# Kernel tuning notes

Measured on AMD Instinct MI355X. Metric: run time of the kernel, lower is better.

Reference implementation:

```python
import jax, jax.numpy as jnp
import numpy as np

N, E = 50000, 1600000
FEAT, HID, HEADS = 256, 64, 2
NEG_SLOPE = 0.2


def gat_conv(x, src, dst, W, att_src, att_dst, bias, heads, out_ch):
    """PyG GATConv (concat=True, self-loops already appended to src/dst)."""
    n = x.shape[0]
    h = (x @ W).reshape(n, heads, out_ch)                      # [N,H,C]
    a_src = jnp.einsum('nhc,hc->nh', h, att_src)               # [N,H]
    a_dst = jnp.einsum('nhc,hc->nh', h, att_dst)               # [N,H]
    alpha = jax.nn.leaky_relu(a_src[src] + a_dst[dst], NEG_SLOPE)  # [E',H]
    # segment softmax over incoming edges of each dst node
    amax = jax.ops.segment_max(alpha, dst, num_segments=n)
    alpha = jnp.exp(alpha - amax[dst])
    denom = jax.ops.segment_sum(alpha, dst, num_segments=n)
    alpha = alpha / (denom[dst] + 1e-16)
    msg = h[src] * alpha[..., None]                            # [E',H,C]
    out = jax.ops.segment_sum(msg, dst, num_segments=n)        # [N,H,C]
    return out.reshape(n, heads * out_ch) + bias


def setup_inputs() -> dict:
    key = jax.random.key(0)
    ks = jax.random.split(key, 10)
    x = jax.random.normal(ks[0], (N, FEAT), dtype=jnp.float32)
    edge_index = jax.random.randint(ks[1], (2, E), 0, N, dtype=jnp.int64)
    s1 = 1.0 / np.sqrt(FEAT)
    s2 = 1.0 / np.sqrt(HID * HEADS)
    sa = 1.0 / np.sqrt(HID)
    return {
        'x': x,
        'edge_index': edge_index,
        'W1': jax.random.uniform(ks[2], (FEAT, HEADS * HID), jnp.float32, -s1, s1),
        'att_src1': jax.random.uniform(ks[3], (HEADS, HID), jnp.float32, -sa, sa),
        'att_dst1': jax.random.uniform(ks[4], (HEADS, HID), jnp.float32, -sa, sa),
        'b1': jnp.zeros((HEADS * HID,), jnp.float32),
        'W2': jax.random.uniform(ks[5], (HEADS * HID, HID), jnp.float32, -s2, s2),
        'att_src2': jax.random.uniform(ks[6], (1, HID), jnp.float32, -sa, sa),
        'att_dst2': jax.random.uniform(ks[7], (1, HID), jnp.float32, -sa, sa),
        'b2': jnp.zeros((HID,), jnp.float32),
    }


def reference(x, edge_index, W1, att_src1, att_dst1, b1, W2, att_src2, att_dst2, b2):
    n = x.shape[0]
    loop = jnp.arange(n, dtype=edge_index.dtype)
    src = jnp.concatenate([edge_index[0], loop])   # add self loops (PyG default)
    dst = jnp.concatenate([edge_index[1], loop])
    h = gat_conv(x, src, dst, W1, att_src1, att_dst1, b1, HEADS, HID)
    h = jax.nn.relu(h)  # dropout is identity in eval mode
    h = gat_conv(h, src, dst, W2, att_src2, att_dst2, b2, 1, HID)
    return jax.nn.log_softmax(h, axis=1)
```

## Files before the change

### kernel.cpp

```cpp
#include <hip/hip_runtime.h>
#include <hip/hip_bf16.h>
#include <math.h>

typedef short bf16x8 __attribute__((ext_vector_type(8)));
typedef float f32x4 __attribute__((ext_vector_type(4)));

#define BSHIFT 7
#define BWIDTH 128
#define PCHUNK 4096

__global__ void prep_kernel(int* __restrict__ bcnt,
                            const float* __restrict__ W1, const float* __restrict__ W2,
                            __hip_bfloat16* __restrict__ W1t,
                            __hip_bfloat16* __restrict__ W2t) {
    if (blockIdx.x == 0) {
        bcnt[threadIdx.x] = 0;
        bcnt[threadIdx.x + 256] = 0;
        return;
    }
    int idx = (blockIdx.x - 1) * 256 + threadIdx.x;
    const int n1 = 128 * 256;
    if (idx < n1) {
        int nn = idx >> 8, kk = idx & 255;
        W1t[idx] = __float2bfloat16(W1[kk * 128 + nn]);
    } else {
        int j = idx - n1;
        if (j < 64 * 128) {
            int nn = j >> 7, kk = j & 127;
            W2t[j] = __float2bfloat16(W2[kk * 64 + nn]);
        }
    }
}

__global__ __launch_bounds__(256) void bucket_hist(const int* __restrict__ ei, int E,
                                                   int* __restrict__ bcnt) {
    __shared__ int h[512];
    int tid = threadIdx.x;
    for (int i = tid; i < 512; i += 256) h[i] = 0;
    __syncthreads();
    int start = blockIdx.x * PCHUNK;
    int cnt = min(PCHUNK, E - start);
    for (int i = tid; i < cnt; i += 256)
        atomicAdd(&h[ei[E + start + i] >> BSHIFT], 1);
    __syncthreads();
    for (int i = tid; i < 512; i += 256)
        if (h[i]) atomicAdd(&bcnt[i], h[i]);
}

__global__ __launch_bounds__(512) void bucket_scan(const int* __restrict__ bcnt,
                                                   int* __restrict__ bbase,
                                                   int* __restrict__ bcur,
                                                   int nbk, int n) {
    __shared__ int s[512];
    int tid = threadIdx.x;
    int nodes = 0;
    if (tid < nbk) nodes = min(BWIDTH, n - (tid << BSHIFT));
    int v = (tid < nbk) ? bcnt[tid] + nodes : 0;
    s[tid] = v;
    __syncthreads();
    #pragma unroll
    for (int o = 1; o < 512; o <<= 1) {
        int t = (tid >= o) ? s[tid - o] : 0;
        __syncthreads();
        s[tid] += t;
        __syncthreads();
    }
    if (tid < nbk) {
        int ex = s[tid] - v;
        bbase[tid] = ex;
        bcur[tid] = ex - (tid << BSHIFT);
    }
    if (tid == nbk) bbase[nbk] = s[tid];
}

__global__ __launch_bounds__(256) void partition_edges(const int* __restrict__ ei, int E,
                                                       int* __restrict__ bcur,
                                                       int* __restrict__ tmp) {
    __shared__ int2 stage[PCHUNK];
    __shared__ int h[512];
    __shared__ int lbase[512];
    int tid = threadIdx.x;
    int start = blockIdx.x * PCHUNK;
    int cnt = min(PCHUNK, E - start);
    for (int i = tid; i < 512; i += 256) h[i] = 0;
    __syncthreads();
    for (int i = tid; i < cnt; i += 256) {
        int s = ei[start + i];
        int d = ei[E + start + i];
        stage[i] = make_int2(s, d);
        atomicAdd(&h[d >> BSHIFT], 1);
    }
    __syncthreads();
    for (int i = tid; i < 512; i += 256) {
        if (h[i] > 0) lbase[i] = atomicAdd(&bcur[i], h[i]);
        h[i] = 0;
    }
    __syncthreads();
    for (int i = tid; i < cnt; i += 256) {
        int2 e = stage[i];
        int b = e.y >> BSHIFT;
        int r = atomicAdd(&h[b], 1);
        tmp[lbase[b] + r] = (e.x << BSHIFT) | (e.y & (BWIDTH - 1));
    }
}

__global__ __launch_bounds__(256) void bucket_csr(const int* __restrict__ bbase,
                                                  const int* __restrict__ tmp,
                                                  int* __restrict__ offs,
                                                  int* __restrict__ srcs,
                                                  int n, int nbk) {
    __shared__ int cnt[BWIDTH];
    __shared__ int sa[BWIDTH];
    __shared__ int cur[BWIDTH];
    int b = blockIdx.x;
    int tid = threadIdx.x;
    int node0 = b << BSHIFT;
    int nnodes = min(BWIDTH, n - node0);
    int cb = bbase[b];
    int ce = bbase[b + 1];
    int tb = cb - node0;
    int ecnt = (ce - cb) - nnodes;

    if (tid < BWIDTH) cnt[tid] = (tid < nnodes) ? 1 : 0;
    __syncthreads();
    for (int i = tid; i < ecnt; i += 256)
        atomicAdd(&cnt[tmp[tb + i] & (BWIDTH - 1)], 1);
    __syncthreads();
    if (tid < BWIDTH) sa[tid] = cnt[tid];
    __syncthreads();
    #pragma unroll
    for (int o = 1; o < BWIDTH; o <<= 1) {
        int v = 0;
        if (tid < BWIDTH) { v = sa[tid]; if (tid >= o) v += sa[tid - o]; }
        __syncthreads();
        if (tid < BWIDTH) sa[tid] = v;
        __syncthreads();
    }
    if (tid < BWIDTH) {
        int ex = sa[tid] - cnt[tid];
        if (tid < nnodes) {
            offs[node0 + tid] = cb + ex;
            srcs[cb + ex] = node0 + tid;
        }
        cur[tid] = ex + (tid < nnodes ? 1 : 0);
    }
    if (b == nbk - 1 && tid == 0) offs[n] = ce;
    __syncthreads();
    for (int i = tid; i < ecnt; i += 256) {
        int e = tmp[tb + i];
        int li = e & (BWIDTH - 1);
        int r = atomicAdd(&cur[li], 1);
        srcs[cb + r] = e >> BSHIFT;
    }
}

template <bool A_BF16, int NT, int HEADS>
__global__ __launch_bounds__(256) void gemm_att(
    const void* __restrict__ Av, const __hip_bfloat16* __restrict__ Bt,
    __hip_bfloat16* __restrict__ C,
    const float* __restrict__ atts, const float* __restrict__ attd,
    float* __restrict__ a_s, float* __restrict__ a_d, int M, int K) {
    constexpr int N = NT * 16;
    __shared__ __hip_bfloat16 As[64][40];
    int tid = threadIdx.x;
    int w = tid >> 6, l = tid & 63;
    int q = l >> 4, m16 = l & 15;
    int bm = blockIdx.x * 64;

    int lr = tid >> 2, lseg = tid & 3;
    int arow = bm + lr; if (arow >= M) arow = M - 1;

    f32x4 acc[NT];
    #pragma unroll
    for (int t = 0; t < NT; t++) acc[t] = (f32x4){0.f, 0.f, 0.f, 0.f};

    for (int kc = 0; kc < K; kc += 32) {
        if (A_BF16) {
            const __hip_bfloat16* A = (const __hip_bfloat16*)Av;
            uint4 v = *(const uint4*)(A + (size_t)arow * K + kc + lseg * 8);
            *(uint4*)&As[lr][lseg * 8] = v;
        } else {
            const float* A = (const float*)Av;
            float4 v0 = *(const float4*)(A + (size_t)arow * K + kc + lseg * 8);
            float4 v1 = *(const float4*)(A + (size_t)arow * K + kc + lseg * 8 + 4);
            union { __hip_bfloat16 h[8]; uint4 u; } tmp;
            tmp.h[0] = __float2bfloat16(v0.x); tmp.h[1] = __float2bfloat16(v0.y);
            tmp.h[2] = __float2bfloat16(v0.z); tmp.h[3] = __float2bfloat16(v0.w);
            tmp.h[4] = __float2bfloat16(v1.x); tmp.h[5] = __float2bfloat16(v1.y);
            tmp.h[6] = __float2bfloat16(v1.z); tmp.h[7] = __float2bfloat16(v1.w);
            *(uint4*)&As[lr][lseg * 8] = tmp.u;
        }
        __syncthreads();
        bf16x8 a = *(const bf16x8*)&As[w * 16 + m16][q * 8];
        #pragma unroll
        for (int t = 0; t < NT; t++) {
            bf16x8 b = *(const bf16x8*)(Bt + (size_t)(t * 16 + m16) * K + kc + q * 8);
            acc[t] = __builtin_amdgcn_mfma_f32_16x16x32_bf16(a, b, acc[t], 0, 0, 0);
        }
        __syncthreads();
    }

    #pragma unroll
    for (int t = 0; t < NT; t++) {
        #pragma unroll
        for (int r = 0; r < 4; r++) {
            int row = bm + w * 16 + q * 4 + r;
            if (row < M) C[(size_t)row * N + t * 16 + m16] = __float2bfloat16(acc[t][r]);
        }
    }

    float ps[HEADS][4], pd[HEADS][4];
    #pragma unroll
    for (int hh = 0; hh < HEADS; hh++)
        #pragma unroll
        for (int r = 0; r < 4; r++) { ps[hh][r] = 0.f; pd[hh][r] = 0.f; }
    #pragma unroll
    for (int t = 0; t < NT; t++) {
        int ch = t * 16 + m16;
        float asw = atts[ch], adw = attd[ch];
        int hh = (HEADS == 2) ? (t >> 2) : 0;
        #pragma unroll
        for (int r = 0; r < 4; r++) {
            ps[hh][r] = fmaf(acc[t][r], asw, ps[hh][r]);
            pd[hh][r] = fmaf(acc[t][r], adw, pd[hh][r]);
        }
    }
    #pragma unroll
    for (int o = 1; o < 16; o <<= 1) {
        #pragma unroll
        for (int hh = 0; hh < HEADS; hh++)
            #pragma unroll
            for (int r = 0; r < 4; r++) {
                ps[hh][r] += __shfl_xor(ps[hh][r], o);
                pd[hh][r] += __shfl_xor(pd[hh][r], o);
            }
    }
    if (m16 == 0) {
        #pragma unroll
        for (int r = 0; r < 4; r++) {
            int row = bm + w * 16 + q * 4 + r;
            if (row < M) {
                if (HEADS == 2) {
                    a_s[row * 2]     = ps[0][r];
                    a_s[row * 2 + 1] = ps[1][r];
                    a_d[row * 2]     = pd[0][r];
                    a_d[row * 2 + 1] = pd[1][r];
                } else {
                    a_s[row] = ps[0][r];
                    a_d[row] = pd[0][r];
                }
            }
        }
    }
}

__device__ __forceinline__ float leaky(float r) {
    return r < 0.f ? 0.2f * r : r;
}

__device__ __forceinline__ void unpack2(unsigned u, float& lo, float& hi) {
    lo = __uint_as_float(u << 16);
    hi = __uint_as_float(u & 0xffff0000u);
}

__global__ __launch_bounds__(256) void edge_agg_l1(
    const int* __restrict__ offs, const int* __restrict__ srcs,
    const __hip_bfloat16* __restrict__ h1, const float* __restrict__ asv,
    const float* __restrict__ adv, const float* __restrict__ bias,
    __hip_bfloat16* __restrict__ out, int n) {
    int d = (blockIdx.x * blockDim.x + threadIdx.x) >> 6;
    int lane = threadIdx.x & 63;
    if (d >= n) return;
    int start = offs[d], end = offs[d + 1];
    float ad0 = adv[2 * d], ad1 = adv[2 * d + 1];

    int sub = lane & 15;
    int g = lane >> 4;
    int ch0 = sub * 8;
    int hsel = sub >> 3;

    float s0 = 0.f, s1 = 0.f;
    float acc[8];
    #pragma unroll
    for (int k = 0; k < 8; k++) acc[k] = 0.f;

    for (int base = start; base < end; base += 64) {
        int cnt = min(64, end - base);
        int s_l = 0;
        float e0 = 0.f, e1 = 0.f;
        if (lane < cnt) {
            s_l = srcs[base + lane];
            float2 a = *(const float2*)(asv + 2 * s_l);
            e0 = __expf(leaky(a.x + ad0));
            e1 = __expf(leaky(a.y + ad1));
        }
        s0 += e0;
        s1 += e1;

        int steps = (cnt + 3) >> 2;
        int jj = 0;
        for (; jj + 2 <= steps; jj += 2) {
            int eA = jj * 4 + g, eB = eA + 4;
            float w0A = __shfl(e0, eA), w1A = __shfl(e1, eA);
            int sA = __shfl(s_l, eA);
            float w0B = __shfl(e0, eB), w1B = __shfl(e1, eB);
            int sB = __shfl(s_l, eB);
            float wA = hsel ? w1A : w0A;
            float wB = hsel ? w1B : w0B;
            uint4 vA = *(const uint4*)(h1 + (size_t)sA * 128 + ch0);
            uint4 vB = *(const uint4*)(h1 + (size_t)sB * 128 + ch0);
            float f0, f1, f2, f3, f4, f5, f6, f7;
            unpack2(vA.x, f0, f1); unpack2(vA.y, f2, f3);
            unpack2(vA.z, f4, f5); unpack2(vA.w, f6, f7);
            acc[0] = fmaf(wA, f0, acc[0]); acc[1] = fmaf(wA, f1, acc[1]);
            acc[2] = fmaf(wA, f2, acc[2]); acc[3] = fmaf(wA, f3, acc[3]);
            acc[4] = fmaf(wA, f4, acc[4]); acc[5] = fmaf(wA, f5, acc[5]);
            acc[6] = fmaf(wA, f6, acc[6]); acc[7] = fmaf(wA, f7, acc[7]);
            unpack2(vB.x, f0, f1); unpack2(vB.y, f2, f3);
            unpack2(vB.z, f4, f5); unpack2(vB.w, f6, f7);
            acc[0] = fmaf(wB, f0, acc[0]); acc[1] = fmaf(wB, f1, acc[1]);
            acc[2] = fmaf(wB, f2, acc[2]); acc[3] = fmaf(wB, f3, acc[3]);
            acc[4] = fmaf(wB, f4, acc[4]); acc[5] = fmaf(wB, f5, acc[5]);
            acc[6] = fmaf(wB, f6, acc[6]); acc[7] = fmaf(wB, f7, acc[7]);
        }
        if (jj < steps) {
            int eA = jj * 4 + g;
            float w0A = __shfl(e0, eA), w1A = __shfl(e1, eA);
            int sA = __shfl(s_l, eA);
            float wA = hsel ? w1A : w0A;
            uint4 vA = *(const uint4*)(h1 + (size_t)sA * 128 + ch0);
            float f0, f1, f2, f3, f4, f5, f6, f7;
            unpack2(vA.x, f0, f1); unpack2(vA.y, f2, f3);
            unpack2(vA.z, f4, f5); unpack2(vA.w, f6, f7);
            acc[0] = fmaf(wA, f0, acc[0]); acc[1] = fmaf(wA, f1, acc[1]);
            acc[2] = fmaf(wA, f2, acc[2]); acc[3] = fmaf(wA, f3, acc[3]);
            acc[4] = fmaf(wA, f4, acc[4]); acc[5] = fmaf(wA, f5, acc[5]);
            acc[6] = fmaf(wA, f6, acc[6]); acc[7] = fmaf(wA, f7, acc[7]);
        }
    }
    #pragma unroll
    for (int o = 16; o < 64; o <<= 1)
        #pragma unroll
        for (int k = 0; k < 8; k++) acc[k] += __shfl_xor(acc[k], o);
    #pragma unroll
    for (int o = 1; o < 64; o <<= 1) {
        s0 += __shfl_xor(s0, o);
        s1 += __shfl_xor(s1, o);
    }

    if (lane < 16) {
        float invh = 1.f / ((hsel ? s1 : s0) + 1e-16f);
        float4 b0 = *(const float4*)(bias + ch0);
        float4 b1 = *(const float4*)(bias + ch0 + 4);
        union { __hip_bfloat16 h[8]; uint4 u; } o2;
        o2.h[0] = __float2bfloat16(fmaxf(fmaf(acc[0], invh, b0.x), 0.f));
        o2.h[1] = __float2bfloat16(fmaxf(fmaf(acc[1], invh, b0.y), 0.f));
        o2.h[2] = __float2bfloat16(fmaxf(fmaf(acc[2], invh, b0.z), 0.f));
        o2.h[3] = __float2bfloat16(fmaxf(fmaf(acc[3], invh, b0.w), 0.f));
        o2.h[4] = __float2bfloat16(fmaxf(fmaf(acc[4], invh, b1.x), 0.f));
        o2.h[5] = __float2bfloat16(fmaxf(fmaf(acc[5], invh, b1.y), 0.f));
        o2.h[6] = __float2bfloat16(fmaxf(fmaf(acc[6], invh, b1.z), 0.f));
        o2.h[7] = __float2bfloat16(fmaxf(fmaf(acc[7], invh, b1.w), 0.f));
        *(uint4*)(out + (size_t)d * 128 + ch0) = o2.u;
    }
}

__global__ __launch_bounds__(256) void edge_agg_l2(
    const int* __restrict__ offs, const int* __restrict__ srcs,
    const __hip_bfloat16* __restrict__ h2, const float* __restrict__ asv,
    const float* __restrict__ adv, const float* __restrict__ bias,
    float* __restrict__ out, int n) {
    int d = (blockIdx.x * blockDim.x + threadIdx.x) >> 6;
    int lane = threadIdx.x & 63;
    if (d >= n) return;
    int start = offs[d], end = offs[d + 1];
    float ad = adv[d];

    int sub = lane & 7;
    int g = lane >> 3;
    int ch0 = sub * 8;

    float ssum = 0.f;
    float acc[8];
    #pragma unroll
    for (int k = 0; k < 8; k++) acc[k] = 0.f;

    for (int base = start; base < end; base += 64) {
        int cnt = min(64, end - base);
        int s_l = 0;
        float ew = 0.f;
        if (lane < cnt) {
            s_l = srcs[base + lane];
            ew = __expf(leaky(asv[s_l] + ad));
        }
        ssum += ew;

        int steps = (cnt + 7) >> 3;
        int jj = 0;
        for (; jj + 2 <= steps; jj += 2) {
            int eA = jj * 8 + g, eB = eA + 8;
            float wA = __shfl(ew, eA);
            int sA = __shfl(s_l, eA);
            float wB = __shfl(ew, eB);
            int sB = __shfl(s_l, eB);
            uint4 vA = *(const uint4*)(h2 + (size_t)sA * 64 + ch0);
            uint4 vB = *(const uint4*)(h2 + (size_t)sB * 64 + ch0);
            float f0, f1, f2, f3, f4, f5, f6, f7;
            unpack2(vA.x, f0, f1); unpack2(vA.y, f2, f3);
            unpack2(vA.z, f4, f5); unpack2(vA.w, f6, f7);
            acc[0] = fmaf(wA, f0, acc[0]); acc[1] = fmaf(wA, f1, acc[1]);
            acc[2] = fmaf(wA, f2, acc[2]); acc[3] = fmaf(wA, f3, acc[3]);
            acc[4] = fmaf(wA, f4, acc[4]); acc[5] = fmaf(wA, f5, acc[5]);
            acc[6] = fmaf(wA, f6, acc[6]); acc[7] = fmaf(wA, f7, acc[7]);
            unpack2(vB.x, f0, f1); unpack2(vB.y, f2, f3);
            unpack2(vB.z, f4, f5); unpack2(vB.w, f6, f7);
            acc[0] = fmaf(wB, f0, acc[0]); acc[1] = fmaf(wB, f1, acc[1]);
            acc[2] = fmaf(wB, f2, acc[2]); acc[3] = fmaf(wB, f3, acc[3]);
            acc[4] = fmaf(wB, f4, acc[4]); acc[5] = fmaf(wB, f5, acc[5]);
            acc[6] = fmaf(wB, f6, acc[6]); acc[7] = fmaf(wB, f7, acc[7]);
        }
        if (jj < steps) {
            int eA = jj * 8 + g;
            float wA = __shfl(ew, eA);
            int sA = __shfl(s_l, eA);
            uint4 vA = *(const uint4*)(h2 + (size_t)sA * 64 + ch0);
            float f0, f1, f2, f3, f4, f5, f6, f7;
            unpack2(vA.x, f0, f1); unpack2(vA.y, f2, f3);
            unpack2(vA.z, f4, f5); unpack2(vA.w, f6, f7);
            acc[0] = fmaf(wA, f0, acc[0]); acc[1] = fmaf(wA, f1, acc[1]);
            acc[2] = fmaf(wA, f2, acc[2]); acc[3] = fmaf(wA, f3, acc[3]);
            acc[4] = fmaf(wA, f4, acc[4]); acc[5] = fmaf(wA, f5, acc[5]);
            acc[6] = fmaf(wA, f6, acc[6]); acc[7] = fmaf(wA, f7, acc[7]);
        }
    }
    #pragma unroll
    for (int o = 8; o < 64; o <<= 1)
        #pragma unroll
        for (int k = 0; k < 8; k++) acc[k] += __shfl_xor(acc[k], o);
    #pragma unroll
    for (int o = 1; o < 64; o <<= 1) ssum += __shfl_xor(ssum, o);

    float inv = 1.f / (ssum + 1e-16f);
    float4 b0 = *(const float4*)(bias + ch0);
    float4 b1 = *(const float4*)(bias + ch0 + 4);
    float v[8];
    v[0] = fmaf(acc[0], inv, b0.x); v[1] = fmaf(acc[1], inv, b0.y);
    v[2] = fmaf(acc[2], inv, b0.z); v[3] = fmaf(acc[3], inv, b0.w);
    v[4] = fmaf(acc[4], inv, b1.x); v[5] = fmaf(acc[5], inv, b1.y);
    v[6] = fmaf(acc[6], inv, b1.z); v[7] = fmaf(acc[7], inv, b1.w);

    float vm = v[0];
    #pragma unroll
    for (int k = 1; k < 8; k++) vm = fmaxf(vm, v[k]);
    #pragma unroll
    for (int o = 1; o < 8; o <<= 1) vm = fmaxf(vm, __shfl_xor(vm, o));
    float se_loc = 0.f;
    #pragma unroll
    for (int k = 0; k < 8; k++) se_loc += __expf(v[k] - vm);
    #pragma unroll
    for (int o = 1; o < 8; o <<= 1) se_loc += __shfl_xor(se_loc, o);
    float lse = vm + logf(se_loc);

    if (lane < 8) {
        float4 o0 = make_float4(v[0] - lse, v[1] - lse, v[2] - lse, v[3] - lse);
        float4 o1 = make_float4(v[4] - lse, v[5] - lse, v[6] - lse, v[7] - lse);
        *(float4*)(out + (size_t)d * 64 + ch0) = o0;
        *(float4*)(out + (size_t)d * 64 + ch0 + 4) = o1;
    }
}

extern "C" void kernel_launch(void* const* d_in, const int* in_sizes, int n_in,
                              void* d_out, int out_size, void* d_ws, size_t ws_size,
                              hipStream_t stream) {
    const float* x    = (const float*)d_in[0];
    const int*   ei   = (const int*)d_in[1];
    const float* W1   = (const float*)d_in[2];
    const float* as1w = (const float*)d_in[3];
    const float* ad1w = (const float*)d_in[4];
    const float* b1   = (const float*)d_in[5];
    const float* W2   = (const float*)d_in[6];
    const float* as2w = (const float*)d_in[7];
    const float* ad2w = (const float*)d_in[8];
    const float* b2   = (const float*)d_in[9];
    float* out = (float*)d_out;

    const int n = in_sizes[0] / 256;
    const int E = in_sizes[1] / 2;
    const int tot = E + n;
    const int nbk = (n + BWIDTH - 1) / BWIDTH;

    char* p = (char*)d_ws;
    auto alloc = [&](size_t bytes) {
        void* r = (void*)p;
        p += (bytes + 255) & ~(size_t)255;
        return r;
    };
    int*   offs  = (int*)alloc((size_t)(n + 1) * 4);
    int*   srcs  = (int*)alloc((size_t)tot * 4);
    int*   tmp   = (int*)alloc((size_t)E * 4);
    int*   bcnt  = (int*)alloc(512 * 4);
    int*   bbase = (int*)alloc(512 * 4);
    int*   bcur  = (int*)alloc(512 * 4);
    __hip_bfloat16* W1t = (__hip_bfloat16*)alloc((size_t)128 * 256 * 2);
    __hip_bfloat16* W2t = (__hip_bfloat16*)alloc((size_t)64 * 128 * 2);
    __hip_bfloat16* h1  = (__hip_bfloat16*)alloc((size_t)n * 128 * 2);
    __hip_bfloat16* out1= (__hip_bfloat16*)alloc((size_t)n * 128 * 2);
    __hip_bfloat16* h2  = (__hip_bfloat16*)alloc((size_t)n * 64 * 2);
    float* a_s1 = (float*)alloc((size_t)n * 2 * 4);
    float* a_d1 = (float*)alloc((size_t)n * 2 * 4);
    float* a_s2 = (float*)alloc((size_t)n * 4);
    float* a_d2 = (float*)alloc((size_t)n * 4);

    int pblocks = (E + PCHUNK - 1) / PCHUNK;

    prep_kernel<<<1 + (128 * 256 + 64 * 128 + 255) / 256, 256, 0, stream>>>(
        bcnt, W1, W2, W1t, W2t);

    bucket_hist<<<pblocks, 256, 0, stream>>>(ei, E, bcnt);
    bucket_scan<<<1, 512, 0, stream>>>(bcnt, bbase, bcur, nbk, n);
    partition_edges<<<pblocks, 256, 0, stream>>>(ei, E, bcur, tmp);
    bucket_csr<<<nbk, 256, 0, stream>>>(bbase, tmp, offs, srcs, n, nbk);

    gemm_att<false, 8, 2><<<(n + 63) / 64, 256, 0, stream>>>(
        x, W1t, h1, as1w, ad1w, a_s1, a_d1, n, 256);
    edge_agg_l1<<<((size_t)n * 64 + 255) / 256, 256, 0, stream>>>(
        offs, srcs, h1, a_s1, a_d1, b1, out1, n);

    gemm_att<true, 4, 1><<<(n + 63) / 64, 256, 0, stream>>>(
        out1, W2t, h2, as2w, ad2w, a_s2, a_d2, n, 128);
    edge_agg_l2<<<((size_t)n * 64 + 255) / 256, 256, 0, stream>>>(
        offs, srcs, h2, a_s2, a_d2, b2, out, n);
}
```

Before: 285.0 us.

## Precompute edge attention weights in separate edge-parallel kernels before aggregation

Moves the per-edge exp(leaky(a_src+a_dst)) computation out of the per-node aggregation kernels into new flat edge-parallel kernels, which read a dst array now emitted by the CSR build. It also packs src/dst into a single 16-bit/16-bit int in partition staging, which allows a PCHUNK of 8192. The bcnt zeroing moves to a memset. The aim is to take the gather-plus-exp latency off the aggregation warps, at the cost of extra kernel launches and an extra write and read of the weight and dst arrays. The 16-bit packing only holds while node ids stay below 65536.

```diff
diff --git a/kernel.cpp b/kernel.cpp
--- a/kernel.cpp
+++ b/kernel.cpp
@@ -7,18 +7,12 @@
 
 #define BSHIFT 7
 #define BWIDTH 128
-#define PCHUNK 4096
-
-__global__ void prep_kernel(int* __restrict__ bcnt,
-                            const float* __restrict__ W1, const float* __restrict__ W2,
-                            __hip_bfloat16* __restrict__ W1t,
-                            __hip_bfloat16* __restrict__ W2t) {
-    if (blockIdx.x == 0) {
-        bcnt[threadIdx.x] = 0;
-        bcnt[threadIdx.x + 256] = 0;
-        return;
-    }
-    int idx = (blockIdx.x - 1) * 256 + threadIdx.x;
+#define PCHUNK 8192
+
+__global__ void transpose_both(const float* __restrict__ W1, const float* __restrict__ W2,
+                               __hip_bfloat16* __restrict__ W1t,
+                               __hip_bfloat16* __restrict__ W2t) {
+    int idx = blockIdx.x * blockDim.x + threadIdx.x;
     const int n1 = 128 * 256;
     if (idx < n1) {
         int nn = idx >> 8, kk = idx & 255;
@@ -76,7 +70,7 @@
 __global__ __launch_bounds__(256) void partition_edges(const int* __restrict__ ei, int E,
                                                        int* __restrict__ bcur,
                                                        int* __restrict__ tmp) {
-    __shared__ int2 stage[PCHUNK];
+    __shared__ int stage[PCHUNK];
     __shared__ int h[512];
     __shared__ int lbase[512];
     int tid = threadIdx.x;
@@ -87,7 +81,7 @@
     for (int i = tid; i < cnt; i += 256) {
         int s = ei[start + i];
         int d = ei[E + start + i];
-        stage[i] = make_int2(s, d);
+        stage[i] = (s << 16) | d;
         atomicAdd(&h[d >> BSHIFT], 1);
     }
     __syncthreads();
@@ -97,10 +91,10 @@
     }
     __syncthreads();
     for (int i = tid; i < cnt; i += 256) {
-        int2 e = stage[i];
-        int b = e.y >> BSHIFT;
+        int e = stage[i];
+        int b = (e & 0xffff) >> BSHIFT;
         int r = atomicAdd(&h[b], 1);
-        tmp[lbase[b] + r] = (e.x << BSHIFT) | (e.y & (BWIDTH - 1));
+        tmp[lbase[b] + r] = e;
     }
 }
 
@@ -108,6 +102,7 @@
                                                   const int* __restrict__ tmp,
                                                   int* __restrict__ offs,
                                                   int* __restrict__ srcs,
+                                                  int* __restrict__ dsts,
                                                   int n, int nbk) {
     __shared__ int cnt[BWIDTH];
     __shared__ int sa[BWIDTH];
@@ -141,6 +136,7 @@
         if (tid < nnodes) {
             offs[node0 + tid] = cb + ex;
             srcs[cb + ex] = node0 + tid;
+            dsts[cb + ex] = node0 + tid;
         }
         cur[tid] = ex + (tid < nnodes ? 1 : 0);
     }
@@ -150,8 +146,34 @@
         int e = tmp[tb + i];
         int li = e & (BWIDTH - 1);
         int r = atomicAdd(&cur[li], 1);
-        srcs[cb + r] = e >> BSHIFT;
-    }
+        srcs[cb + r] = ((unsigned)e) >> 16;
+        dsts[cb + r] = node0 + li;
+    }
+}
+
+__device__ __forceinline__ float leaky(float r) {
+    return r < 0.f ? 0.2f * r : r;
+}
+
+__global__ __launch_bounds__(256) void ew1_kernel(
+    const int* __restrict__ srcs, const int* __restrict__ dsts,
+    const float* __restrict__ asv, const float* __restrict__ adv,
+    float2* __restrict__ w, int tot) {
+    int i = blockIdx.x * blockDim.x + threadIdx.x;
+    if (i >= tot) return;
+    int s = srcs[i], d = dsts[i];
+    float2 a = ((const float2*)asv)[s];
+    float2 ad = ((const float2*)adv)[d];
+    w[i] = make_float2(__expf(leaky(a.x + ad.x)), __expf(leaky(a.y + ad.y)));
+}
+
+__global__ __launch_bounds__(256) void ew2_kernel(
+    const int* __restrict__ srcs, const int* __restrict__ dsts,
+    const float* __restrict__ asv, const float* __restrict__ adv,
+    float* __restrict__ w, int tot) {
+    int i = blockIdx.x * blockDim.x + threadIdx.x;
+    if (i >= tot) return;
+    w[i] = __expf(leaky(asv[srcs[i]] + adv[dsts[i]]));
 }
 
 template <bool A_BF16, int NT, int HEADS>
@@ -254,10 +276,6 @@
     }
 }
 
-__device__ __forceinline__ float leaky(float r) {
-    return r < 0.f ? 0.2f * r : r;
-}
-
 __device__ __forceinline__ void unpack2(unsigned u, float& lo, float& hi) {
     lo = __uint_as_float(u << 16);
     hi = __uint_as_float(u & 0xffff0000u);
@@ -265,14 +283,12 @@
 
 __global__ __launch_bounds__(256) void edge_agg_l1(
     const int* __restrict__ offs, const int* __restrict__ srcs,
-    const __hip_bfloat16* __restrict__ h1, const float* __restrict__ asv,
-    const float* __restrict__ adv, const float* __restrict__ bias,
-    __hip_bfloat16* __restrict__ out, int n) {
+    const float2* __restrict__ wv1, const __hip_bfloat16* __restrict__ h1,
+    const float* __restrict__ bias, __hip_bfloat16* __restrict__ out, int n) {
     int d = (blockIdx.x * blockDim.x + threadIdx.x) >> 6;
     int lane = threadIdx.x & 63;
     if (d >= n) return;
     int start = offs[d], end = offs[d + 1];
-    float ad0 = adv[2 * d], ad1 = adv[2 * d + 1];
 
     int sub = lane & 15;
     int g = lane >> 4;
@@ -287,23 +303,21 @@
     for (int base = start; base < end; base += 64) {
         int cnt = min(64, end - base);
         int s_l = 0;
-        float e0 = 0.f, e1 = 0.f;
+        float2 wl = make_float2(0.f, 0.f);
         if (lane < cnt) {
             s_l = srcs[base + lane];
-            float2 a = *(const float2*)(asv + 2 * s_l);
-            e0 = __expf(leaky(a.x + ad0));
-            e1 = __expf(leaky(a.y + ad1));
-        }
-        s0 += e0;
-        s1 += e1;
+            wl = wv1[base + lane];
+        }
+        s0 += wl.x;
+        s1 += wl.y;
 
         int steps = (cnt + 3) >> 2;
         int jj = 0;
         for (; jj + 2 <= steps; jj += 2) {
             int eA = jj * 4 + g, eB = eA + 4;
-            float w0A = __shfl(e0, eA), w1A = __shfl(e1, eA);
+            float w0A = __shfl(wl.x, eA), w1A = __shfl(wl.y, eA);
             int sA = __shfl(s_l, eA);
-            float w0B = __shfl(e0, eB), w1B = __shfl(e1, eB);
+            float w0B = __shfl(wl.x, eB), w1B = __shfl(wl.y, eB);
             int sB = __shfl(s_l, eB);
             float wA = hsel ? w1A : w0A;
             float wB = hsel ? w1B : w0B;
@@ -325,7 +339,7 @@
         }
         if (jj < steps) {
             int eA = jj * 4 + g;
-            float w0A = __shfl(e0, eA), w1A = __shfl(e1, eA);
+            float w0A = __shfl(wl.x, eA), w1A = __shfl(wl.y, eA);
             int sA = __shfl(s_l, eA);
             float wA = hsel ? w1A : w0A;
             uint4 vA = *(const uint4*)(h1 + (size_t)sA * 128 + ch0);
@@ -367,14 +381,12 @@
 
 __global__ __launch_bounds__(256) void edge_agg_l2(
     const int* __restrict__ offs, const int* __restrict__ srcs,
-    const __hip_bfloat16* __restrict__ h2, const float* __restrict__ asv,
-    const float* __restrict__ adv, const float* __restrict__ bias,
-    float* __restrict__ out, int n) {
+    const float* __restrict__ wv2, const __hip_bfloat16* __restrict__ h2,
+    const float* __restrict__ bias, float* __restrict__ out, int n) {
     int d = (blockIdx.x * blockDim.x + threadIdx.x) >> 6;
     int lane = threadIdx.x & 63;
     if (d >= n) return;
     int start = offs[d], end = offs[d + 1];
-    float ad = adv[d];
 
     int sub = lane & 7;
     int g = lane >> 3;
@@ -391,7 +403,7 @@
         float ew = 0.f;
         if (lane < cnt) {
             s_l = srcs[base + lane];
-            ew = __expf(leaky(asv[s_l] + ad));
+            ew = wv2[base + lane];
         }
         ssum += ew;
 
@@ -497,7 +509,10 @@
     };
     int*   offs  = (int*)alloc((size_t)(n + 1) * 4);
     int*   srcs  = (int*)alloc((size_t)tot * 4);
+    int*   dsts  = (int*)alloc((size_t)tot * 4);
     int*   tmp   = (int*)alloc((size_t)E * 4);
+    float2* wv1  = (float2*)alloc((size_t)tot * 8);
+    float* wv2   = (float*)alloc((size_t)tot * 4);
     int*   bcnt  = (int*)alloc(512 * 4);
     int*   bbase = (int*)alloc(512 * 4);
     int*   bcur  = (int*)alloc(512 * 4);
@@ -513,21 +528,23 @@
 
     int pblocks = (E + PCHUNK - 1) / PCHUNK;
 
-    prep_kernel<<<1 + (128 * 256 + 64 * 128 + 255) / 256, 256, 0, stream>>>(
-        bcnt, W1, W2, W1t, W2t);
+    hipMemsetAsync(bcnt, 0, 512 * 4, stream);
+    transpose_both<<<(128 * 256 + 64 * 128 + 255) / 256, 256, 0, stream>>>(W1, W2, W1t, W2t);
 
     bucket_hist<<<pblocks, 256, 0, stream>>>(ei, E, bcnt);
     bucket_scan<<<1, 512, 0, stream>>>(bcnt, bbase, bcur, nbk, n);
     partition_edges<<<pblocks, 256, 0, stream>>>(ei, E, bcur, tmp);
-    bucket_csr<<<nbk, 256, 0, stream>>>(bbase, tmp, offs, srcs, n, nbk);
+    bucket_csr<<<nbk, 256, 0, stream>>>(bbase, tmp, offs, srcs, dsts, n, nbk);
 
     gemm_att<false, 8, 2><<<(n + 63) / 64, 256, 0, stream>>>(
         x, W1t, h1, as1w, ad1w, a_s1, a_d1, n, 256);
+    ew1_kernel<<<(tot + 255) / 256, 256, 0, stream>>>(srcs, dsts, a_s1, a_d1, wv1, tot);
     edge_agg_l1<<<((size_t)n * 64 + 255) / 256, 256, 0, stream>>>(
-        offs, srcs, h1, a_s1, a_d1, b1, out1, n);
+        offs, srcs, wv1, h1, b1, out1, n);
 
     gemm_att<true, 4, 1><<<(n + 63) / 64, 256, 0, stream>>>(
         out1, W2t, h2, as2w, ad2w, a_s2, a_d2, n, 128);
+    ew2_kernel<<<(tot + 255) / 256, 256, 0, stream>>>(srcs, dsts, a_s2, a_d2, wv2, tot);
     edge_agg_l2<<<((size_t)n * 64 + 255) / 256, 256, 0, stream>>>(
-        offs, srcs, h2, a_s2, a_d2, b2, out, n);
-}
+        offs, srcs, wv2, h2, b2, out, n);
+}
```

Measured after the change: 311.5 us. +9.3%, slower.
